# Optimization experiments

Measured on AMD Instinct MI355X. Metric: run time of the kernel, lower is better.

Reference implementation:

```python
import jax, jax.numpy as jnp
import numpy as np

B, L, CH = 8, 32768, 128   # segments, points per segment, channels
H, D = 4, 32               # num_head, ch_head (CH == H*D)
EPS = 1e-5                 # torch GroupNorm default eps


def group_norm1(x, w, b):
    # GroupNorm(num_groups=1, num_channels=CH) applied on [1, CH, L] per segment:
    # normalize over all channels AND points of each segment, then per-channel affine.
    mu = jnp.mean(x, axis=(1, 2), keepdims=True)            # [B,1,1]
    var = jnp.var(x, axis=(1, 2), keepdims=True)            # [B,1,1]
    return (x - mu) * jax.lax.rsqrt(var + EPS) * w + b      # [B,L,CH]


def setup_inputs() -> dict:
    key = jax.random.key(0)
    k0, k1, k2 = jax.random.split(key, 3)
    x = jax.random.normal(k0, (B, L, CH), dtype=jnp.float32)
    W_qkv = jax.random.normal(k1, (CH, 3 * H * D), dtype=jnp.float32) * 0.02
    W_out = jax.random.normal(k2, (H * D, CH), dtype=jnp.float32) * 0.02
    gn1_w = jnp.ones((CH,), jnp.float32)
    gn1_b = jnp.zeros((CH,), jnp.float32)
    gn2_w = jnp.ones((CH,), jnp.float32)
    gn2_b = jnp.zeros((CH,), jnp.float32)
    return {"x": x, "gn1_w": gn1_w, "gn1_b": gn1_b, "W_qkv": W_qkv,
            "W_out": W_out, "gn2_w": gn2_w, "gn2_b": gn2_b}


def reference(x, gn1_w, gn1_b, W_qkv, W_out, gn2_w, gn2_b):
    norm_x = group_norm1(x, gn1_w, gn1_b)                     # [B,L,CH]
    qkv = norm_x @ W_qkv                                      # [B,L,3*H*D]
    q, k, v = jnp.split(qkv, 3, axis=-1)
    q = q.reshape(B, L, H, D)
    k = k.reshape(B, L, H, D)
    v = v.reshape(B, L, H, D)
    # softmax over points within each segment (k / sqrt(segment_len))
    k_soft = jax.nn.softmax(k * (1.0 / np.float32(np.sqrt(L))), axis=1)
    # per-segment, per-head KV context: [B,H,D,D]
    context = jnp.einsum('blhk,blhv->bhkv', k_soft, v)
    # q scaled by ch_head**-0.5, softmax over feature dim
    q_soft = jax.nn.softmax(q * np.float32(D ** -0.5), axis=-1)
    out = jnp.einsum('blhk,bhkv->blhv', q_soft, context).reshape(B, L, H * D)
    out = out @ W_out                                          # [B,L,CH]
    out = group_norm1(out, gn2_w, gn2_b)
    return out + x  # residual
```

## Files before the change

### kernel.cpp

```cpp
#include <hip/hip_runtime.h>

#define NSEG 8
#define LSEG 32768
#define EPS_GN 1e-5f
#define KSCALE 0.005524271728019903f
#define QSCALE 0.17677669529663687f
#define INVN 2.384185791015625e-07f
#define SOPITCH 260

typedef __attribute__((ext_vector_type(4))) float f32x4;
typedef __attribute__((ext_vector_type(8))) __bf16 bf16x8;
typedef __attribute__((ext_vector_type(4))) short s16x4;

#define MFMA32(A, B, C) __builtin_amdgcn_mfma_f32_16x16x32_bf16(A, B, C, 0, 0, 0)
#define MFMA16(A, B, C) __builtin_amdgcn_mfma_f32_16x16x16bf16_1k(A, B, C, 0, 0, 0)

static __device__ __forceinline__ unsigned short f2bf(float f) {
  unsigned int u = __float_as_uint(f);
  u += 0x7fffu + ((u >> 16) & 1u);
  return (unsigned short)(u >> 16);
}
static __device__ __forceinline__ float bf2f(unsigned short s) {
  return __uint_as_float(((unsigned int)s) << 16);
}
static __device__ __forceinline__ s16x4 pack4(float a, float b, float c, float d) {
  union { __bf16 h[4]; s16x4 s; } u;
  u.h[0] = (__bf16)a; u.h[1] = (__bf16)b; u.h[2] = (__bf16)c; u.h[3] = (__bf16)d;
  return u.s;
}
static __device__ __forceinline__ ushort4 cvt4(float4 v) {
  union { __bf16 h[4]; ushort4 u; } z;
  z.h[0] = (__bf16)v.x; z.h[1] = (__bf16)v.y; z.h[2] = (__bf16)v.z; z.h[3] = (__bf16)v.w;
  return z.u;
}

__global__ __launch_bounds__(256) void k_pre(
    const float* __restrict__ x, float* __restrict__ part, unsigned short* __restrict__ xb,
    const float* __restrict__ W, const float* __restrict__ gn1w, unsigned short* __restrict__ WT)
{
  const int t = threadIdx.x;
  if (blockIdx.x >= 512) {
    int idx = (blockIdx.x - 512) * 256 + t;
    int n = idx >> 7, ch = idx & 127;
    WT[idx] = f2bf(gn1w[ch] * W[ch * 384 + n]);
    return;
  }
  const int c = blockIdx.x;
  const float4* xp = (const float4*)x + (size_t)c * 16384;
  ushort4* xo = (ushort4*)xb + (size_t)c * 16384;
  float s = 0.f, q = 0.f;
  #pragma unroll 8
  for (int i = 0; i < 64; ++i) {
    float4 v = xp[t + i * 256];
    s += v.x + v.y + v.z + v.w;
    q += v.x*v.x + v.y*v.y + v.z*v.z + v.w*v.w;
    xo[t + i * 256] = cvt4(v);
  }
  #pragma unroll
  for (int o = 1; o < 64; o <<= 1) { s += __shfl_xor(s, o); q += __shfl_xor(q, o); }
  __shared__ float red[8];
  int wave = t >> 6, lane = t & 63;
  if (lane == 0) { red[wave*2] = s; red[wave*2+1] = q; }
  __syncthreads();
  if (t == 0) {
    part[c*2]   = red[0] + red[2] + red[4] + red[6];
    part[c*2+1] = red[1] + red[3] + red[5] + red[7];
  }
}

__global__ __launch_bounds__(256, 2) void k_kv(
    const unsigned short* __restrict__ xb, const unsigned short* __restrict__ WT,
    const float* __restrict__ Wqkv, const float* __restrict__ gn1w, const float* __restrict__ gn1b,
    const float* __restrict__ part, float* __restrict__ sume_p, float* __restrict__ ctx_p)
{
  __shared__ float sm[2];
  __shared__ float sb01[512];
  __shared__ float sbias[256];

  const int t = threadIdx.x;
  const int h = t >> 6, lane = t & 63;
  const int lm = lane & 15, lg = lane >> 4;
  const int bid = blockIdx.x;
  const int seg = bid >> 6, sub = bid & 63;

  if (t < 64) {
    float s = part[(seg*64 + t)*2], q = part[(seg*64 + t)*2 + 1];
    #pragma unroll
    for (int o = 1; o < 64; o <<= 1) { s += __shfl_xor(s, o); q += __shfl_xor(q, o); }
    if (t == 0) {
      float mu = s * INVN;
      float var = q * INVN - mu * mu;
      float rs = rsqrtf(var + EPS_GN);
      sm[0] = mu * rs; sm[1] = rs;
    }
  }
  for (int p = t; p < 512; p += 256) {
    int which = p >> 8, n = 128 + (p & 255);
    const float* gv = which ? gn1w : gn1b;
    float s = 0.f;
    for (int ch = 0; ch < 128; ++ch) s += gv[ch] * Wqkv[ch*384 + n];
    sb01[p] = s;
  }
  __syncthreads();
  {
    float mu_rs = sm[0];
    int p = t;
    float v = sb01[p] - mu_rs * sb01[256 + p];
    sbias[p] = v * ((p < 128) ? KSCALE : 1.f);
  }
  __syncthreads();

  const float rs = sm[1];
  const float alk = rs * KSCALE, alv = rs;
  const float ck0 = sbias[h*32 + lm],       ck1 = sbias[h*32 + 16 + lm];
  const float cv0 = sbias[128 + h*32 + lm], cv1 = sbias[128 + h*32 + 16 + lm];

  bf16x8 wk[2][4], wv[2][4];
  #pragma unroll
  for (int nt = 0; nt < 2; ++nt)
    #pragma unroll
    for (int kk = 0; kk < 4; ++kk) {
      int row = h*32 + nt*16 + lm;
      wk[nt][kk] = *(const bf16x8*)&WT[(row + 128) * 128 + kk*32 + lg*8];
      wv[nt][kk] = *(const bf16x8*)&WT[(row + 256) * 128 + kk*32 + lg*8];
    }

  f32x4 ctx00 = {0,0,0,0}, ctx01 = {0,0,0,0}, ctx10 = {0,0,0,0}, ctx11 = {0,0,0,0};
  float se0 = 0.f, se1 = 0.f;

  const unsigned short* xw = xb + (size_t)(seg * LSEG + sub*512 + lm) * 128 + lg*8;

#define ISSUE(S, IT) { \
    const unsigned short* p_ = xw + (size_t)((IT) * 16) * 128; \
    S[0] = *(const bf16x8*)(p_);      \
    S[1] = *(const bf16x8*)(p_ + 32); \
    S[2] = *(const bf16x8*)(p_ + 64); \
    S[3] = *(const bf16x8*)(p_ + 96); }

#define COMPUTE(S) { \
    f32x4 ka0 = {0,0,0,0}, ka1 = {0,0,0,0}, va0 = {0,0,0,0}, va1 = {0,0,0,0}; \
    _Pragma("unroll") for (int kk = 0; kk < 4; ++kk) { \
      ka0 = MFMA32(S[kk], wk[0][kk], ka0); \
      ka1 = MFMA32(S[kk], wk[1][kk], ka1); \
    } \
    _Pragma("unroll") for (int kk = 0; kk < 4; ++kk) { \
      va0 = MFMA32(S[kk], wv[0][kk], va0); \
      va1 = MFMA32(S[kk], wv[1][kk], va1); \
    } \
    float e_[8]; \
    _Pragma("unroll") for (int r = 0; r < 4; ++r) { \
      e_[r]     = __expf(fmaf(ka0[r], alk, ck0)); \
      e_[4 + r] = __expf(fmaf(ka1[r], alk, ck1)); \
    } \
    se0 += (e_[0] + e_[1]) + (e_[2] + e_[3]); \
    se1 += (e_[4] + e_[5]) + (e_[6] + e_[7]); \
    s16x4 E0 = pack4(e_[0], e_[1], e_[2], e_[3]); \
    s16x4 E1 = pack4(e_[4], e_[5], e_[6], e_[7]); \
    s16x4 V0 = pack4(fmaf(va0[0], alv, cv0), fmaf(va0[1], alv, cv0), \
                     fmaf(va0[2], alv, cv0), fmaf(va0[3], alv, cv0)); \
    s16x4 V1 = pack4(fmaf(va1[0], alv, cv1), fmaf(va1[1], alv, cv1), \
                     fmaf(va1[2], alv, cv1), fmaf(va1[3], alv, cv1)); \
    ctx00 = MFMA16(E0, V0, ctx00); \
    ctx01 = MFMA16(E0, V1, ctx01); \
    ctx10 = MFMA16(E1, V0, ctx10); \
    ctx11 = MFMA16(E1, V1, ctx11); }

  bf16x8 sA[4], sB[4];
  ISSUE(sA, 0);
  #pragma unroll 1
  for (int it = 0; it < 32; it += 2) {
    ISSUE(sB, it + 1);
    COMPUTE(sA);
    if (it + 2 < 32) ISSUE(sA, it + 2);
    COMPUTE(sB);
  }
#undef ISSUE
#undef COMPUTE

  se0 += __shfl_xor(se0, 16); se0 += __shfl_xor(se0, 32);
  se1 += __shfl_xor(se1, 16); se1 += __shfl_xor(se1, 32);
  if (lane < 16) {
    sume_p[(size_t)bid*128 + h*32 + lm]      = se0;
    sume_p[(size_t)bid*128 + h*32 + 16 + lm] = se1;
  }
  float* cp = ctx_p + (size_t)bid*4096 + h*1024;
  #pragma unroll
  for (int r = 0; r < 4; ++r) {
    cp[(lg*4 + r)*32      + lm]      = ctx00[r];
    cp[(lg*4 + r)*32      + 16 + lm] = ctx01[r];
    cp[(16 + lg*4 + r)*32 + lm]      = ctx10[r];
    cp[(16 + lg*4 + r)*32 + 16 + lm] = ctx11[r];
  }
}

__global__ __launch_bounds__(256) void k_wc(
    const float* __restrict__ sume_p, const float* __restrict__ ctx_p,
    const float* __restrict__ Wout, unsigned short* __restrict__ WcT)
{
  __shared__ float sctx[1024];
  __shared__ float sse[32];
  const int t = threadIdx.x, b = blockIdx.x;
  const int seg = b >> 5, head = (b >> 3) & 3, ocg = b & 7;
  float acc[4] = {0.f, 0.f, 0.f, 0.f};
  for (int j = 0; j < 64; ++j) {
    const float* cp = ctx_p + (size_t)(seg*64 + j)*4096 + head*1024;
    #pragma unroll
    for (int e = 0; e < 4; ++e) acc[e] += cp[t + e*256];
  }
  if (t < 32) {
    float s = 0.f;
    for (int j = 0; j < 64; ++j) s += sume_p[(size_t)(seg*64 + j)*128 + head*32 + t];
    sse[t] = s;
  }
  #pragma unroll
  for (int e = 0; e < 4; ++e) sctx[t + e*256] = acc[e];
  __syncthreads();
  #pragma unroll
  for (int e = 0; e < 2; ++e) {
    int idx = t + e*256;
    int kc = idx >> 4, ocl = idx & 15;
    int oc = ocg*16 + ocl;
    float s = 0.f;
    #pragma unroll
    for (int vc = 0; vc < 32; ++vc)
      s += sctx[kc*32 + vc] * Wout[(head*32 + vc)*128 + oc];
    WcT[((size_t)seg*128 + oc)*128 + head*32 + kc] = f2bf(s / sse[kc]);
  }
}

__global__ __launch_bounds__(256, 2) void k_out3(
    const unsigned short* __restrict__ xb, const unsigned short* __restrict__ WT,
    const float* __restrict__ Wqkv, const float* __restrict__ gn1w, const float* __restrict__ gn1b,
    const float* __restrict__ part, const unsigned short* __restrict__ WcT,
    float* __restrict__ part2, unsigned short* __restrict__ outm)
{
  __shared__ float sm[2];
  __shared__ float sb01[256];
  __shared__ float sbq[128];
  __shared__ float red[8];
  __shared__ __attribute__((aligned(16))) short pbuf[2][8 * 256];
  __shared__ __attribute__((aligned(16))) unsigned short sou[2][16 * SOPITCH];

  const int t = threadIdx.x;
  const int w = t >> 6, lane = t & 63;
  const int lm = lane & 15, lg = lane >> 4;
  const int bid = blockIdx.x;
  const int seg = bid >> 6;
  const size_t cb = (size_t)bid * 512;

  if (t < 64) {
    float s = part[(seg*64 + t)*2], q = part[(seg*64 + t)*2 + 1];
    #pragma unroll
    for (int o = 1; o < 64; o <<= 1) { s += __shfl_xor(s, o); q += __shfl_xor(q, o); }
    if (t == 0) {
      float mu = s * INVN;
      float var = q * INVN - mu * mu;
      float rs = rsqrtf(var + EPS_GN);
      sm[0] = mu * rs; sm[1] = rs;
    }
  }
  {
    int which = t >> 7, n = t & 127;
    const float* gv = which ? gn1w : gn1b;
    float s = 0.f;
    for (int ch = 0; ch < 128; ++ch) s += gv[ch] * Wqkv[ch*384 + n];
    sb01[t] = s;
  }
  __syncthreads();
  if (t < 128) sbq[t] = (sb01[t] - sm[0] * sb01[128 + t]) * QSCALE;
  __syncthreads();

  const float alq = sm[1] * QSCALE;
  const float4 cq0 = *(const float4*)&sbq[w*32 + lg*4];
  const float4 cq1 = *(const float4*)&sbq[w*32 + 16 + lg*4];

  bf16x8 wq[2][4];
  #pragma unroll
  for (int nt = 0; nt < 2; ++nt)
    #pragma unroll
    for (int kk = 0; kk < 4; ++kk)
      wq[nt][kk] = *(const bf16x8*)&WT[(w*32 + nt*16 + lm) * 128 + kk*32 + lg*8];
  s16x4 wc[2][8];
  #pragma unroll
  for (int o = 0; o < 2; ++o)
    #pragma unroll
    for (int kt = 0; kt < 8; ++kt)
      wc[o][kt] = *(const s16x4*)&WcT[((size_t)seg*128 + (w*32 + o*16 + lm))*128 + kt*16 + lg*4];

  const unsigned short* xw = xb + (cb + lm) * 128 + lg*8;
  float ssum = 0.f, ssq = 0.f;
  bf16x8 xf0, xf1, xf2, xf3;

#define LOADXF(IT) { \
    const unsigned short* p_ = xw + (size_t)((IT) * 16) * 128; \
    xf0 = *(const bf16x8*)(p_);      \
    xf1 = *(const bf16x8*)(p_ + 32); \
    xf2 = *(const bf16x8*)(p_ + 64); \
    xf3 = *(const bf16x8*)(p_ + 96); }

#define SM2P(D) { \
    f32x4 qa0 = {0,0,0,0}, qa1 = {0,0,0,0}; \
    qa0 = MFMA32(wq[0][0], xf0, qa0); qa1 = MFMA32(wq[1][0], xf0, qa1); \
    qa0 = MFMA32(wq[0][1], xf1, qa0); qa1 = MFMA32(wq[1][1], xf1, qa1); \
    qa0 = MFMA32(wq[0][2], xf2, qa0); qa1 = MFMA32(wq[1][2], xf2, qa1); \
    qa0 = MFMA32(wq[0][3], xf3, qa0); qa1 = MFMA32(wq[1][3], xf3, qa1); \
    float a_[8]; \
    _Pragma("unroll") for (int r = 0; r < 4; ++r) { \
      a_[r]     = fmaf(qa0[r], alq, ((const float*)&cq0)[r]); \
      a_[4 + r] = fmaf(qa1[r], alq, ((const float*)&cq1)[r]); \
    } \
    float m_ = a_[0]; \
    _Pragma("unroll") for (int i = 1; i < 8; ++i) m_ = fmaxf(m_, a_[i]); \
    m_ = fmaxf(m_, __shfl_xor(m_, 16)); \
    m_ = fmaxf(m_, __shfl_xor(m_, 32)); \
    float s_ = 0.f; \
    _Pragma("unroll") for (int i = 0; i < 8; ++i) { a_[i] = __expf(a_[i] - m_); s_ += a_[i]; } \
    s_ += __shfl_xor(s_, 16); \
    s_ += __shfl_xor(s_, 32); \
    float inv_ = 1.f / s_; \
    *(s16x4*)&pbuf[D][(w*2)*256 + lane*4]     = pack4(a_[0]*inv_, a_[1]*inv_, a_[2]*inv_, a_[3]*inv_); \
    *(s16x4*)&pbuf[D][(w*2 + 1)*256 + lane*4] = pack4(a_[4]*inv_, a_[5]*inv_, a_[6]*inv_, a_[7]*inv_); }

  LOADXF(0);
  SM2P(0);

  #pragma unroll 1
  for (int ia = 0; ia < 32; ++ia) {
    const int d = ia & 1;
    __syncthreads();
    if (ia + 1 < 32) LOADXF(ia + 1);
    f32x4 acc0 = {0,0,0,0}, acc1 = {0,0,0,0};
    #pragma unroll
    for (int kt = 0; kt < 8; ++kt) {
      s16x4 pk = *(const s16x4*)&pbuf[d][kt*256 + lane*4];
      acc0 = MFMA16(wc[0][kt], pk, acc0);
      acc1 = MFMA16(wc[1][kt], pk, acc1);
    }
    if (ia > 0) {
      #pragma unroll
      for (int j = 0; j < 2; ++j) {
        int f = t + j*256;
        int pt = f >> 5, cc = f & 31;
        ((ushort4*)outm)[(cb + (size_t)(ia-1)*16 + pt)*32 + cc] =
            *(const ushort4*)&sou[d^1][pt*SOPITCH + cc*4];
      }
    }
    #pragma unroll
    for (int r = 0; r < 4; ++r) {
      ssum += acc0[r] + acc1[r];
      ssq  += acc0[r]*acc0[r] + acc1[r]*acc1[r];
    }
    {
      unsigned short* dst = &sou[d][lm*SOPITCH + w*32 + lg*4];
      dst[0] = f2bf(acc0[0]); dst[1] = f2bf(acc0[1]);
      dst[2] = f2bf(acc0[2]); dst[3] = f2bf(acc0[3]);
      dst += 16;
      dst[0] = f2bf(acc1[0]); dst[1] = f2bf(acc1[1]);
      dst[2] = f2bf(acc1[2]); dst[3] = f2bf(acc1[3]);
    }
    if (ia + 1 < 32) SM2P(d ^ 1);
  }
  __syncthreads();
  #pragma unroll
  for (int j = 0; j < 2; ++j) {
    int f = t + j*256;
    int pt = f >> 5, cc = f & 31;
    ((ushort4*)outm)[(cb + (size_t)31*16 + pt)*32 + cc] =
        *(const ushort4*)&sou[1][pt*SOPITCH + cc*4];
  }
#undef LOADXF
#undef SM2P

  #pragma unroll
  for (int o = 1; o < 64; o <<= 1) { ssum += __shfl_xor(ssum, o); ssq += __shfl_xor(ssq, o); }
  if (lane == 0) { red[w*2] = ssum; red[w*2+1] = ssq; }
  __syncthreads();
  if (t == 0) {
    part2[bid*2]   = red[0] + red[2] + red[4] + red[6];
    part2[bid*2+1] = red[1] + red[3] + red[5] + red[7];
  }
}

__global__ __launch_bounds__(256) void k_fin(
    const unsigned short* __restrict__ xb, const unsigned short* __restrict__ out_ws,
    const float* __restrict__ part2, const float* __restrict__ gn2w, const float* __restrict__ gn2b,
    float* __restrict__ y)
{
  __shared__ float sm[2];
  const int t = threadIdx.x;
  const int b = blockIdx.x >> 8, blk = blockIdx.x & 255;
  if (t < 64) {
    float s = part2[(b*64 + t)*2], q = part2[(b*64 + t)*2 + 1];
    #pragma unroll
    for (int o = 1; o < 64; o <<= 1) { s += __shfl_xor(s, o); q += __shfl_xor(q, o); }
    if (t == 0) {
      float mu = s * INVN;
      float var = q * INVN - mu * mu;
      sm[0] = mu; sm[1] = rsqrtf(var + EPS_GN);
    }
  }
  __syncthreads();
  const float mu = sm[0], rs = sm[1];
  const int c4 = t & 31;
  const float4 w4 = *(const float4*)&gn2w[c4*4];
  const float4 g4 = *(const float4*)&gn2b[c4*4];
  const size_t base = (size_t)b * 1048576 + (size_t)blk * 4096;
  const ushort4* xp = (const ushort4*)xb + base;
  const ushort4* op = (const ushort4*)out_ws + base;
  float4* yp = (float4*)y + base;
  #pragma unroll
  for (int i = 0; i < 16; ++i) {
    int f = t + i * 256;
    ushort4 xv = xp[f];
    ushort4 ov = op[f];
    float4 r;
    r.x = (bf2f(ov.x) - mu) * rs * w4.x + g4.x + bf2f(xv.x);
    r.y = (bf2f(ov.y) - mu) * rs * w4.y + g4.y + bf2f(xv.y);
    r.z = (bf2f(ov.z) - mu) * rs * w4.z + g4.z + bf2f(xv.z);
    r.w = (bf2f(ov.w) - mu) * rs * w4.w + g4.w + bf2f(xv.w);
    yp[f] = r;
  }
}

extern "C" void kernel_launch(void* const* d_in, const int* in_sizes, int n_in,
                              void* d_out, int out_size, void* d_ws, size_t ws_size,
                              hipStream_t stream) {
  const float* x    = (const float*)d_in[0];
  const float* gn1w = (const float*)d_in[1];
  const float* gn1b = (const float*)d_in[2];
  const float* Wqkv = (const float*)d_in[3];
  const float* Wout = (const float*)d_in[4];
  const float* gn2w = (const float*)d_in[5];
  const float* gn2b = (const float*)d_in[6];
  float* y = (float*)d_out;
  char* ws = (char*)d_ws;

  float*          part   = (float*)(ws + 0);
  float*          part2  = (float*)(ws + 4096);
  unsigned short* WT     = (unsigned short*)(ws + 8192);
  unsigned short* WcT    = (unsigned short*)(ws + 106496);
  float*          sume_p = (float*)(ws + 368640);
  float*          ctx_p  = (float*)(ws + 630784);
  unsigned short* xb     = (unsigned short*)(ws + 9019392);
  unsigned short* outm   = (unsigned short*)(ws + 76128256);

  hipLaunchKernelGGL(k_pre,  dim3(704),  dim3(256), 0, stream, x, part, xb, Wqkv, gn1w, WT);
  hipLaunchKernelGGL(k_kv,   dim3(512),  dim3(256), 0, stream, xb, WT, Wqkv, gn1w, gn1b, part, sume_p, ctx_p);
  hipLaunchKernelGGL(k_wc,   dim3(256),  dim3(256), 0, stream, sume_p, ctx_p, Wout, WcT);
  hipLaunchKernelGGL(k_out3, dim3(512),  dim3(256), 0, stream, xb, WT, Wqkv, gn1w, gn1b, part, WcT, part2, outm);
  hipLaunchKernelGGL(k_fin,  dim3(2048), dim3(256), 0, stream, xb, outm, part2, gn2w, gn2b, y);
}
```

Baseline: 218.2 us.

## Hoist GN1 bias folding into a per-segment prep kernel and widen k_pre grid

k_pre now uses 2048 blocks of 16 iterations each instead of 512 blocks of 64, which gives the memory-bound pass over x more parallelism. A new tiny k_prep2 kernel reduces the partial statistics once per segment and computes the folded q/k/v biases and scales. k_kv and k_out3 then read these instead of each block recomputing 128-deep dot products over Wqkv plus the statistic reduction. This costs one extra kernel launch and a serial 8-block kernel in the chain.

```diff
diff --git a/kernel.cpp b/kernel.cpp
--- a/kernel.cpp
+++ b/kernel.cpp
@@ -39,18 +39,18 @@
     const float* __restrict__ W, const float* __restrict__ gn1w, unsigned short* __restrict__ WT)
 {
   const int t = threadIdx.x;
-  if (blockIdx.x >= 512) {
-    int idx = (blockIdx.x - 512) * 256 + t;
+  if (blockIdx.x >= 2048) {
+    int idx = (blockIdx.x - 2048) * 256 + t;
     int n = idx >> 7, ch = idx & 127;
     WT[idx] = f2bf(gn1w[ch] * W[ch * 384 + n]);
     return;
   }
   const int c = blockIdx.x;
-  const float4* xp = (const float4*)x + (size_t)c * 16384;
-  ushort4* xo = (ushort4*)xb + (size_t)c * 16384;
+  const float4* xp = (const float4*)x + (size_t)c * 4096;
+  ushort4* xo = (ushort4*)xb + (size_t)c * 4096;
   float s = 0.f, q = 0.f;
-  #pragma unroll 8
-  for (int i = 0; i < 64; ++i) {
+  #pragma unroll
+  for (int i = 0; i < 16; ++i) {
     float4 v = xp[t + i * 256];
     s += v.x + v.y + v.z + v.w;
     q += v.x*v.x + v.y*v.y + v.z*v.z + v.w*v.w;
@@ -68,52 +68,60 @@
   }
 }
 
+__global__ __launch_bounds__(384) void k_prep2(
+    const float* __restrict__ part, const float* __restrict__ Wqkv,
+    const float* __restrict__ gn1w, const float* __restrict__ gn1b,
+    float* __restrict__ biasv, float* __restrict__ alpha)
+{
+  __shared__ float red[8];
+  __shared__ float sm[2];
+  const int seg = blockIdx.x, t = threadIdx.x;
+  const int wave = t >> 6, lane = t & 63;
+  if (t < 256) {
+    float s = part[(seg*256 + t)*2], q = part[(seg*256 + t)*2 + 1];
+    #pragma unroll
+    for (int o = 1; o < 64; o <<= 1) { s += __shfl_xor(s, o); q += __shfl_xor(q, o); }
+    if (lane == 0) { red[wave*2] = s; red[wave*2+1] = q; }
+  }
+  __syncthreads();
+  if (t == 0) {
+    float s = red[0] + red[2] + red[4] + red[6];
+    float q = red[1] + red[3] + red[5] + red[7];
+    float mu = s * INVN;
+    float var = q * INVN - mu * mu;
+    float rs = rsqrtf(var + EPS_GN);
+    sm[0] = mu * rs; sm[1] = rs;
+  }
+  __syncthreads();
+  const float mu_rs = sm[0], rs = sm[1];
+  float s = 0.f;
+  for (int ch = 0; ch < 128; ++ch)
+    s += (gn1b[ch] - mu_rs * gn1w[ch]) * Wqkv[ch * 384 + t];
+  float scale = (t < 128) ? QSCALE : ((t < 256) ? KSCALE : 1.f);
+  biasv[seg*384 + t] = s * scale;
+  if (t == 0) {
+    alpha[seg*4]   = rs * QSCALE;
+    alpha[seg*4+1] = rs * KSCALE;
+    alpha[seg*4+2] = rs;
+  }
+}
+
 __global__ __launch_bounds__(256, 2) void k_kv(
     const unsigned short* __restrict__ xb, const unsigned short* __restrict__ WT,
-    const float* __restrict__ Wqkv, const float* __restrict__ gn1w, const float* __restrict__ gn1b,
-    const float* __restrict__ part, float* __restrict__ sume_p, float* __restrict__ ctx_p)
-{
-  __shared__ float sm[2];
-  __shared__ float sb01[512];
-  __shared__ float sbias[256];
-
+    const float* __restrict__ biasv, const float* __restrict__ alpha,
+    float* __restrict__ sume_p, float* __restrict__ ctx_p)
+{
   const int t = threadIdx.x;
   const int h = t >> 6, lane = t & 63;
   const int lm = lane & 15, lg = lane >> 4;
   const int bid = blockIdx.x;
   const int seg = bid >> 6, sub = bid & 63;
 
-  if (t < 64) {
-    float s = part[(seg*64 + t)*2], q = part[(seg*64 + t)*2 + 1];
-    #pragma unroll
-    for (int o = 1; o < 64; o <<= 1) { s += __shfl_xor(s, o); q += __shfl_xor(q, o); }
-    if (t == 0) {
-      float mu = s * INVN;
-      float var = q * INVN - mu * mu;
-      float rs = rsqrtf(var + EPS_GN);
-      sm[0] = mu * rs; sm[1] = rs;
-    }
-  }
-  for (int p = t; p < 512; p += 256) {
-    int which = p >> 8, n = 128 + (p & 255);
-    const float* gv = which ? gn1w : gn1b;
-    float s = 0.f;
-    for (int ch = 0; ch < 128; ++ch) s += gv[ch] * Wqkv[ch*384 + n];
-    sb01[p] = s;
-  }
-  __syncthreads();
-  {
-    float mu_rs = sm[0];
-    int p = t;
-    float v = sb01[p] - mu_rs * sb01[256 + p];
-    sbias[p] = v * ((p < 128) ? KSCALE : 1.f);
-  }
-  __syncthreads();
-
-  const float rs = sm[1];
-  const float alk = rs * KSCALE, alv = rs;
-  const float ck0 = sbias[h*32 + lm],       ck1 = sbias[h*32 + 16 + lm];
-  const float cv0 = sbias[128 + h*32 + lm], cv1 = sbias[128 + h*32 + 16 + lm];
+  const float alk = alpha[seg*4 + 1], alv = alpha[seg*4 + 2];
+  const float ck0 = biasv[seg*384 + 128 + h*32 + lm];
+  const float ck1 = biasv[seg*384 + 128 + h*32 + 16 + lm];
+  const float cv0 = biasv[seg*384 + 256 + h*32 + lm];
+  const float cv1 = biasv[seg*384 + 256 + h*32 + 16 + lm];
 
   bf16x8 wk[2][4], wv[2][4];
   #pragma unroll
@@ -230,14 +238,11 @@
 
 __global__ __launch_bounds__(256, 2) void k_out3(
     const unsigned short* __restrict__ xb, const unsigned short* __restrict__ WT,
-    const float* __restrict__ Wqkv, const float* __restrict__ gn1w, const float* __restrict__ gn1b,
-    const float* __restrict__ part, const unsigned short* __restrict__ WcT,
+    const float* __restrict__ biasv, const float* __restrict__ alpha,
+    const unsigned short* __restrict__ WcT,
     float* __restrict__ part2, unsigned short* __restrict__ outm)
 {
-  __shared__ float sm[2];
-  __shared__ float sb01[256];
-  __shared__ float sbq[128];
-  __shared__ float red[8];
+  __shared__ float red8[8];
   __shared__ __attribute__((aligned(16))) short pbuf[2][8 * 256];
   __shared__ __attribute__((aligned(16))) unsigned short sou[2][16 * SOPITCH];
 
@@ -248,31 +253,9 @@
   const int seg = bid >> 6;
   const size_t cb = (size_t)bid * 512;
 
-  if (t < 64) {
-    float s = part[(seg*64 + t)*2], q = part[(seg*64 + t)*2 + 1];
-    #pragma unroll
-    for (int o = 1; o < 64; o <<= 1) { s += __shfl_xor(s, o); q += __shfl_xor(q, o); }
-    if (t == 0) {
-      float mu = s * INVN;
-      float var = q * INVN - mu * mu;
-      float rs = rsqrtf(var + EPS_GN);
-      sm[0] = mu * rs; sm[1] = rs;
-    }
-  }
-  {
-    int which = t >> 7, n = t & 127;
-    const float* gv = which ? gn1w : gn1b;
-    float s = 0.f;
-    for (int ch = 0; ch < 128; ++ch) s += gv[ch] * Wqkv[ch*384 + n];
-    sb01[t] = s;
-  }
-  __syncthreads();
-  if (t < 128) sbq[t] = (sb01[t] - sm[0] * sb01[128 + t]) * QSCALE;
-  __syncthreads();
-
-  const float alq = sm[1] * QSCALE;
-  const float4 cq0 = *(const float4*)&sbq[w*32 + lg*4];
-  const float4 cq1 = *(const float4*)&sbq[w*32 + 16 + lg*4];
+  const float alq = alpha[seg*4];
+  const float4 cq0 = *(const float4*)&biasv[seg*384 + w*32 + lg*4];
+  const float4 cq1 = *(const float4*)&biasv[seg*384 + w*32 + 16 + lg*4];
 
   bf16x8 wq[2][4];
   #pragma unroll
@@ -373,11 +356,11 @@
 
   #pragma unroll
   for (int o = 1; o < 64; o <<= 1) { ssum += __shfl_xor(ssum, o); ssq += __shfl_xor(ssq, o); }
-  if (lane == 0) { red[w*2] = ssum; red[w*2+1] = ssq; }
+  if (lane == 0) { red8[w*2] = ssum; red8[w*2+1] = ssq; }
   __syncthreads();
   if (t == 0) {
-    part2[bid*2]   = red[0] + red[2] + red[4] + red[6];
-    part2[bid*2+1] = red[1] + red[3] + red[5] + red[7];
+    part2[bid*2]   = red8[0] + red8[2] + red8[4] + red8[6];
+    part2[bid*2+1] = red8[1] + red8[3] + red8[5] + red8[7];
   }
 }
 
@@ -436,17 +419,20 @@
   char* ws = (char*)d_ws;
 
   float*          part   = (float*)(ws + 0);
-  float*          part2  = (float*)(ws + 4096);
-  unsigned short* WT     = (unsigned short*)(ws + 8192);
-  unsigned short* WcT    = (unsigned short*)(ws + 106496);
-  float*          sume_p = (float*)(ws + 368640);
-  float*          ctx_p  = (float*)(ws + 630784);
-  unsigned short* xb     = (unsigned short*)(ws + 9019392);
-  unsigned short* outm   = (unsigned short*)(ws + 76128256);
-
-  hipLaunchKernelGGL(k_pre,  dim3(704),  dim3(256), 0, stream, x, part, xb, Wqkv, gn1w, WT);
-  hipLaunchKernelGGL(k_kv,   dim3(512),  dim3(256), 0, stream, xb, WT, Wqkv, gn1w, gn1b, part, sume_p, ctx_p);
-  hipLaunchKernelGGL(k_wc,   dim3(256),  dim3(256), 0, stream, sume_p, ctx_p, Wout, WcT);
-  hipLaunchKernelGGL(k_out3, dim3(512),  dim3(256), 0, stream, xb, WT, Wqkv, gn1w, gn1b, part, WcT, part2, outm);
-  hipLaunchKernelGGL(k_fin,  dim3(2048), dim3(256), 0, stream, xb, outm, part2, gn2w, gn2b, y);
-}
+  float*          part2  = (float*)(ws + 16384);
+  unsigned short* WT     = (unsigned short*)(ws + 24576);
+  unsigned short* WcT    = (unsigned short*)(ws + 122880);
+  float*          biasv  = (float*)(ws + 385024);
+  float*          alphav = (float*)(ws + 397312);
+  float*          sume_p = (float*)(ws + 401408);
+  float*          ctx_p  = (float*)(ws + 663552);
+  unsigned short* xb     = (unsigned short*)(ws + 9052160);
+  unsigned short* outm   = (unsigned short*)(ws + 76161024);
+
+  hipLaunchKernelGGL(k_pre,   dim3(2240), dim3(256), 0, stream, x, part, xb, Wqkv, gn1w, WT);
+  hipLaunchKernelGGL(k_prep2, dim3(8),    dim3(384), 0, stream, part, Wqkv, gn1w, gn1b, biasv, alphav);
+  hipLaunchKernelGGL(k_kv,    dim3(512),  dim3(256), 0, stream, xb, WT, biasv, alphav, sume_p, ctx_p);
+  hipLaunchKernelGGL(k_wc,    dim3(256),  dim3(256), 0, stream, sume_p, ctx_p, Wout, WcT);
+  hipLaunchKernelGGL(k_out3,  dim3(512),  dim3(256), 0, stream, xb, WT, biasv, alphav, WcT, part2, outm);
+  hipLaunchKernelGGL(k_fin,   dim3(2048), dim3(256), 0, stream, xb, outm, part2, gn2w, gn2b, y);
+}
```

After: 197.6 us. -9.5%, faster.
